# Kernel optimization log

Hardware: AMD Instinct MI355X
Metric: run time of the kernel (lower is better)

Reference implementation:

```python
import jax, jax.numpy as jnp
import numpy as np

NUM_CODES = 2048
CODE_DEPTH = 64
D_MODEL = 1024
EMA_DECAY = 0.99


def setup_inputs() -> dict:
    key = jax.random.key(0)
    ks = jax.random.split(key, 4)
    x = jax.random.normal(ks[0], (8, 2048, D_MODEL), dtype=jnp.float32)
    # downsampler Linear(d_model, code_depth)
    W_down = jax.random.normal(ks[1], (CODE_DEPTH, D_MODEL), dtype=jnp.float32) / np.sqrt(D_MODEL)
    b_down = jnp.zeros((CODE_DEPTH,), dtype=jnp.float32)
    # codebook: randn, row-normalized, code 0 zeroed (padding code)
    cb = jax.random.normal(ks[2], (1, NUM_CODES, CODE_DEPTH), dtype=jnp.float32)
    cb = cb / jnp.linalg.norm(cb, axis=-1, keepdims=True)
    cb = cb.at[:, 0].set(0.0)
    cluster_sizes = jnp.zeros((1, NUM_CODES), dtype=jnp.float32)
    cluster_sums = jnp.zeros((1, NUM_CODES, CODE_DEPTH), dtype=jnp.float32)
    return {"x": x, "W_down": W_down, "b_down": b_down, "codebook": cb,
            "cluster_sizes": cluster_sizes, "cluster_sums": cluster_sums}


def reference(x, W_down, b_down, codebook, cluster_sizes, cluster_sums):
    """Quantizer.forward, level=0, training=True, quantize=True, mask=None,
    gumbel=False, reverse_ema=False, ema_decay>0."""
    decay = EMA_DECAY
    num_codes = codebook.shape[1]
    cb = codebook[0]                                   # [K, D]
    # downsample + L2 normalize
    z = jnp.einsum('bsm,dm->bsd', x, W_down) + b_down  # [B, S, D]
    z = z / jnp.linalg.norm(z, axis=-1, keepdims=True)
    zd = jax.lax.stop_gradient(z)
    # cdist(z.detach(), codebook[1:]) -> euclidean distances [B, S, K-1]
    codes = cb[1:]
    d2 = (jnp.sum(zd * zd, -1, keepdims=True)
          + jnp.sum(codes * codes, -1)
          - 2.0 * jnp.einsum('bsd,kd->bsk', zd, codes))
    dist = jnp.sqrt(jnp.maximum(d2, 0.0))
    code_indices = jnp.argmin(dist, axis=-1) + 1       # [B, S], in [1, K)
    hard = cb[code_indices]                            # embedding lookup
    # commitment loss: mse(hard.detach(), z)
    commitment_loss = jnp.mean((jax.lax.stop_gradient(hard) - z) ** 2)
    # one-hot aggregation
    onehot = jax.nn.one_hot(code_indices, num_codes, dtype=z.dtype)  # [B,S,K]
    flat_onehot = onehot.reshape(-1, num_codes)        # [N, K]
    bincounts = flat_onehot.sum(axis=0)                # [K]
    used = bincounts != 0                              # [K] bool
    # unused-code loss: mean of per-(batch,code) min distance over unused codes
    code_dist = jnp.min(dist, axis=-2)                 # [B, K-1]
    unused_mask = ~used[1:]                            # [K-1]
    cnt = jnp.sum(unused_mask.astype(jnp.float32)) * code_dist.shape[0]
    unused_code_loss = jnp.sum(code_dist * unused_mask[None, :]) / jnp.maximum(cnt, 1.0)
    # EMA scatter update (forward/standard EMA)
    obs = zd.reshape(-1, zd.shape[-1])                 # [N, D]
    sums = flat_onehot.T @ obs                         # [K, D]
    new_cs = decay * cluster_sizes[0] + (1.0 - decay) * jax.lax.stop_gradient(bincounts)
    new_csum = decay * cluster_sums[0] + (1.0 - decay) * jax.lax.stop_gradient(sums)
    n = new_cs.sum()
    smoothed = (new_cs + 1e-5) * n / (n + num_codes * 1e-5)
    centroids = new_csum / smoothed[:, None]
    new_cb = jnp.where(used[:, None], jax.lax.stop_gradient(centroids), cb)
    new_cb = new_cb.at[0].set(0.0)
    # straight-through estimator
    hard_codes = z + jax.lax.stop_gradient(hard - z)
    embedding_loss = unused_code_loss
    return (hard_codes, code_indices, commitment_loss, embedding_loss,
            new_cb[None], new_cs[None], new_csum[None])
```

## Files before the change

kernel.cpp:

```cpp
#include <hip/hip_runtime.h>

#define NROWS 16384
#define DM    1024
#define CD    64
#define NC    2048
#define KC    2047
#define NB    8
#define DECAY 0.99f

#define K3_BLOCKS 512

#define OUT_HARD   0
#define OUT_IDX    1048576
#define OUT_COMMIT 1064960
#define OUT_EMB    1064961
#define OUT_CB     1064962
#define OUT_CS     1196034
#define OUT_CSUM   1198082

#define WS_Z      0
#define WS_CN2    1048576
#define WS_BINC   1050624
#define WS_SUMS   1052672
#define WS_CDIST  1183744
#define WS_COMMIT 1200120
#define WS_ZN2    1200632
#define WS_N      1217016
#define WS_PART   1298940
#define WS_BV     WS_PART
#define WS_BI     (WS_PART + 65536)

#define F32_INF_BITS 0x7F800000u

__global__ __launch_bounds__(256) void k0_init(const float* __restrict__ cb,
                                               float* __restrict__ ws) {
  int i = blockIdx.x * 256 + threadIdx.x;
  if (i < NC * CD) (ws + WS_SUMS)[i] = 0.0f;
  if (i < NC) {
    ((unsigned*)(ws + WS_BINC))[i] = 0u;
    float cn2;
    if (i < KC) {
      const float* c = cb + (size_t)(i + 1) * CD;
      float s0 = 0.f, s1 = 0.f;
      #pragma unroll
      for (int d = 0; d < CD; d += 2) { s0 = fmaf(c[d], c[d], s0); s1 = fmaf(c[d+1], c[d+1], s1); }
      cn2 = s0 + s1;
    } else {
      cn2 = __uint_as_float(F32_INF_BITS);
    }
    (ws + WS_CN2)[i] = cn2;
  }
  if (i < NB * KC) ((unsigned*)(ws + WS_CDIST))[i] = F32_INF_BITS;
}

__global__ __launch_bounds__(256) void k1_split(const float* __restrict__ x,
                                                const float* __restrict__ W,
                                                float* __restrict__ ws) {
  __shared__ float xs[64][132];
  __shared__ float wls[64][68];
  const int t = threadIdx.x;
  const int ks = blockIdx.x & 3;
  const int row0 = (blockIdx.x >> 2) * 128;
  const int kbase = ks * 256;
  const int tx = t & 15, ty = t >> 4;
  const int sseg = t & 15, srow = t >> 4;

  float4 px[8], pw[4];
  auto ld = [&](int kt) {
    const int kk = kbase + kt * 64;
    #pragma unroll
    for (int it = 0; it < 8; ++it)
      px[it] = *(const float4*)(x + (size_t)(row0 + srow + 16 * it) * DM + kk + sseg * 4);
    #pragma unroll
    for (int it = 0; it < 4; ++it)
      pw[it] = *(const float4*)(W + (size_t)(srow + 16 * it) * DM + kk + sseg * 4);
  };
  ld(0);

  float acc[8][4];
  #pragma unroll
  for (int i = 0; i < 8; i++)
    #pragma unroll
    for (int j = 0; j < 4; j++) acc[i][j] = 0.f;

  for (int kt = 0; kt < 4; ++kt) {
    __syncthreads();
    const int sg4 = sseg * 4;
    #pragma unroll
    for (int it = 0; it < 8; ++it) {
      const int cpos = (srow + 16 * it) ^ ((sseg & 3) << 3);
      xs[sg4 + 0][cpos] = px[it].x; xs[sg4 + 1][cpos] = px[it].y;
      xs[sg4 + 2][cpos] = px[it].z; xs[sg4 + 3][cpos] = px[it].w;
    }
    #pragma unroll
    for (int it = 0; it < 4; ++it) {
      const int wcol = srow + 16 * it;
      wls[sg4 + 0][wcol] = pw[it].x; wls[sg4 + 1][wcol] = pw[it].y;
      wls[sg4 + 2][wcol] = pw[it].z; wls[sg4 + 3][wcol] = pw[it].w;
    }
    __syncthreads();
    if (kt < 3) ld(kt + 1);

    #pragma unroll 8
    for (int dl = 0; dl < 64; ++dl) {
      const int xcol = (ty * 8) ^ (((dl >> 2) & 3) << 3);
      float4 xv0 = *(const float4*)(&xs[dl][xcol]);
      float4 xv1 = *(const float4*)(&xs[dl][xcol + 4]);
      float4 wv  = *(const float4*)(&wls[dl][tx * 4]);
      float xz[8] = {xv0.x, xv0.y, xv0.z, xv0.w, xv1.x, xv1.y, xv1.z, xv1.w};
      float wc[4] = {wv.x, wv.y, wv.z, wv.w};
      #pragma unroll
      for (int i = 0; i < 8; i++)
        #pragma unroll
        for (int j = 0; j < 4; j++)
          acc[i][j] = fmaf(xz[i], wc[j], acc[i][j]);
    }
  }

  float* part = ws + WS_PART + (size_t)ks * NROWS * CD;
  #pragma unroll
  for (int i = 0; i < 8; i++) {
    const int row = row0 + ty * 8 + i;
    float4 v; v.x = acc[i][0]; v.y = acc[i][1]; v.z = acc[i][2]; v.w = acc[i][3];
    *(float4*)(part + (size_t)row * CD + tx * 4) = v;
  }
}

__global__ __launch_bounds__(256) void k1_reduce(const float* __restrict__ bdown,
                                                 float* __restrict__ ws) {
  const int t = threadIdx.x;
  const int tx = t & 15, ty = t >> 4;
  const int row = blockIdx.x * 16 + ty;
  const float* part = ws + WS_PART;
  const size_t off = (size_t)row * CD + tx * 4;

  float4 v0 = *(const float4*)(part + off);
  float4 v1 = *(const float4*)(part + (size_t)1 * NROWS * CD + off);
  float4 v2 = *(const float4*)(part + (size_t)2 * NROWS * CD + off);
  float4 v3 = *(const float4*)(part + (size_t)3 * NROWS * CD + off);
  float4 b  = *(const float4*)(bdown + tx * 4);
  float4 v;
  v.x = (v0.x + v1.x) + (v2.x + v3.x) + b.x;
  v.y = (v0.y + v1.y) + (v2.y + v3.y) + b.y;
  v.z = (v0.z + v1.z) + (v2.z + v3.z) + b.z;
  v.w = (v0.w + v1.w) + (v2.w + v3.w) + b.w;

  float ss = v.x * v.x + v.y * v.y + v.z * v.z + v.w * v.w;
  #pragma unroll
  for (int m = 1; m < 16; m <<= 1) ss += __shfl_xor(ss, m, 64);
  float inv = 1.0f / sqrtf(ss);
  float4 zv; zv.x = v.x * inv; zv.y = v.y * inv; zv.z = v.z * inv; zv.w = v.w * inv;
  *(float4*)(ws + WS_Z + off) = zv;
  if (tx == 0) (ws + WS_ZN2)[row] = ss * inv * inv;
}

__global__ __launch_bounds__(256) void k1_down(const float* __restrict__ x,
                                               const float* __restrict__ W,
                                               const float* __restrict__ bdown,
                                               float* __restrict__ ws) {
  __shared__ float xs[64][68];
  __shared__ float wls[64][68];
  const int t = threadIdx.x;
  const int row0 = blockIdx.x * 64;
  const int tx = t & 15, ty = t >> 4;

  int pr[4], pseg[4];
  #pragma unroll
  for (int it = 0; it < 4; ++it) { int c = t + it * 256; pr[it] = c >> 4; pseg[it] = c & 15; }

  float4 px[4], pw[4];
  #pragma unroll
  for (int it = 0; it < 4; ++it) {
    px[it] = *(const float4*)(x + (size_t)(row0 + pr[it]) * DM + pseg[it] * 4);
    pw[it] = *(const float4*)(W + (size_t)pr[it] * DM + pseg[it] * 4);
  }

  float acc[4][4];
  #pragma unroll
  for (int i = 0; i < 4; i++)
    #pragma unroll
    for (int j = 0; j < 4; j++) acc[i][j] = 0.f;

  for (int kt = 0; kt < 16; ++kt) {
    __syncthreads();
    #pragma unroll
    for (int it = 0; it < 4; ++it) {
      *(float4*)(&xs[pr[it]][pseg[it] * 4]) = px[it];
      *(float4*)(&wls[pr[it]][pseg[it] * 4]) = pw[it];
    }
    __syncthreads();
    if (kt < 15) {
      const int k0 = (kt + 1) * 64;
      #pragma unroll
      for (int it = 0; it < 4; ++it) {
        px[it] = *(const float4*)(x + (size_t)(row0 + pr[it]) * DM + k0 + pseg[it] * 4);
        pw[it] = *(const float4*)(W + (size_t)pr[it] * DM + k0 + pseg[it] * 4);
      }
    }
    #pragma unroll 4
    for (int k = 0; k < 64; k += 4) {
      float4 xv[4], wv[4];
      #pragma unroll
      for (int i = 0; i < 4; i++) xv[i] = *(const float4*)(&xs[ty * 4 + i][k]);
      #pragma unroll
      for (int j = 0; j < 4; j++) wv[j] = *(const float4*)(&wls[tx * 4 + j][k]);
      #pragma unroll
      for (int i = 0; i < 4; i++)
        #pragma unroll
        for (int j = 0; j < 4; j++)
          acc[i][j] = fmaf(xv[i].x, wv[j].x, fmaf(xv[i].y, wv[j].y,
                      fmaf(xv[i].z, wv[j].z, fmaf(xv[i].w, wv[j].w, acc[i][j]))));
    }
  }

  #pragma unroll
  for (int j = 0; j < 4; j++) {
    float bj = bdown[tx * 4 + j];
    #pragma unroll
    for (int i = 0; i < 4; i++) acc[i][j] += bj;
  }

  float* z = ws + WS_Z;
  float* zn2 = ws + WS_ZN2;
  #pragma unroll
  for (int i = 0; i < 4; i++) {
    float ss = acc[i][0] * acc[i][0] + acc[i][1] * acc[i][1] +
               acc[i][2] * acc[i][2] + acc[i][3] * acc[i][3];
    #pragma unroll
    for (int m = 1; m < 16; m <<= 1) ss += __shfl_xor(ss, m, 64);
    float inv = 1.0f / sqrtf(ss);
    float4 zv;
    zv.x = acc[i][0] * inv; zv.y = acc[i][1] * inv;
    zv.z = acc[i][2] * inv; zv.w = acc[i][3] * inv;
    int row = row0 + ty * 4 + i;
    *(float4*)(z + (size_t)row * CD + tx * 4) = zv;
    if (tx == 0) zn2[row] = ss * inv * inv;
  }
}

__global__ __launch_bounds__(512) void k2_dist(const float* __restrict__ cbp,
                                               float* __restrict__ ws) {
  __shared__ float zT[64][132];
  __shared__ float cT[64][132];
  __shared__ float cn2s[128];
  __shared__ float zn2s[128];
  __shared__ unsigned colmin[128];

  const int t = threadIdx.x;
  const int gq = blockIdx.x & 3;
  const int rt = blockIdx.x >> 2;
  const int row0 = rt << 7;
  const int batch = rt >> 4;
  const int tx = t & 31, ty = t >> 5;
  const float* z = ws + WS_Z;
  const float* cn2p = ws + WS_CN2;
  unsigned* cdist = (unsigned*)(ws + WS_CDIST) + (size_t)batch * KC;

  if (t < 128) zn2s[t] = (ws + WS_ZN2)[row0 + t];

  {
    const int sr = t >> 2, sp = t & 3;
    float4 v[4];
    #pragma unroll
    for (int it = 0; it < 4; ++it)
      v[it] = *(const float4*)(z + (size_t)(row0 + sr) * CD + (sp + 4 * it) * 4);
    #pragma unroll
    for (int it = 0; it < 4; ++it) {
      const int sg4 = (sp + 4 * it) * 4;
      zT[sg4 + 0][sr] = v[it].x; zT[sg4 + 1][sr] = v[it].y;
      zT[sg4 + 2][sr] = v[it].z; zT[sg4 + 3][sr] = v[it].w;
    }
  }

  const int cr = t >> 2, cp = t & 3;
  const int ccol = cr ^ (((cr >> 5) & 3) << 2);
  float4 pc[4];
  auto ldc = [&](int lt) {
    const int code = gq * 512 + lt * 128 + cr;
    #pragma unroll
    for (int it = 0; it < 4; ++it)
      pc[it] = (code < KC) ? *(const float4*)(cbp + (size_t)(code + 1) * CD + (cp + 4 * it) * 4)
                           : make_float4(0.f, 0.f, 0.f, 0.f);
  };
  ldc(0);

  float bestv[8];
  int besti[8];
  #pragma unroll
  for (int i = 0; i < 8; i++) { bestv[i] = __uint_as_float(F32_INF_BITS); besti[i] = 0; }

  const int ccol0 = (tx * 4) ^ (((tx >> 3) & 3) << 2);

  for (int lt = 0; lt < 4; ++lt) {
    __syncthreads();
    #pragma unroll
    for (int it = 0; it < 4; ++it) {
      const int sg4 = (cp + 4 * it) * 4;
      cT[sg4 + 0][ccol] = pc[it].x; cT[sg4 + 1][ccol] = pc[it].y;
      cT[sg4 + 2][ccol] = pc[it].z; cT[sg4 + 3][ccol] = pc[it].w;
    }
    if (t < 128) {
      cn2s[t] = cn2p[gq * 512 + lt * 128 + t];
      colmin[t] = F32_INF_BITS;
    }
    __syncthreads();
    if (lt < 3) ldc(lt + 1);

    float acc[8][4];
    #pragma unroll
    for (int i = 0; i < 8; i++)
      #pragma unroll
      for (int j = 0; j < 4; j++) acc[i][j] = 0.f;

    #pragma unroll 8
    for (int d = 0; d < 64; ++d) {
      float4 za = *(const float4*)(&zT[d][ty * 8]);
      float4 zb = *(const float4*)(&zT[d][ty * 8 + 4]);
      float4 cv = *(const float4*)(&cT[d][ccol0]);
      float zz[8] = {za.x, za.y, za.z, za.w, zb.x, zb.y, zb.z, zb.w};
      float cc[4] = {cv.x, cv.y, cv.z, cv.w};
      #pragma unroll
      for (int i = 0; i < 8; i++)
        #pragma unroll
        for (int j = 0; j < 4; j++)
          acc[i][j] = fmaf(zz[i], cc[j], acc[i][j]);
    }

    const int jbase = gq * 512 + lt * 128;
    #pragma unroll
    for (int jl = 0; jl < 4; ++jl) {
      const int jloc = tx * 4 + jl;
      const int jg = jbase + jloc;
      const float c2 = cn2s[jloc];
      float colv = __uint_as_float(F32_INF_BITS);
      #pragma unroll
      for (int i = 0; i < 8; ++i) {
        float s = fmaf(-2.f, acc[i][jl], c2);
        if (s < bestv[i]) { bestv[i] = s; besti[i] = jg; }
        float v = zn2s[ty * 8 + i] + s;
        v = v < 0.f ? 0.f : v;
        colv = v < colv ? v : colv;
      }
      colv = fminf(colv, __shfl_xor(colv, 32, 64));
      if ((t & 32) == 0) atomicMin(&colmin[jloc], __float_as_uint(colv));
    }
    __syncthreads();
    if (t < 128) {
      const int jg2 = jbase + t;
      if (jg2 < KC) atomicMin(&cdist[jg2], colmin[t]);
    }
  }

  #pragma unroll
  for (int m = 1; m <= 16; m <<= 1) {
    #pragma unroll
    for (int i = 0; i < 8; i++) {
      float ov = __shfl_xor(bestv[i], m, 64);
      int oi = __shfl_xor(besti[i], m, 64);
      if (ov < bestv[i] || (ov == bestv[i] && oi < besti[i])) { bestv[i] = ov; besti[i] = oi; }
    }
  }
  if (tx == 0) {
    #pragma unroll
    for (int i = 0; i < 8; i++) {
      const int row = row0 + ty * 8 + i;
      (ws + WS_BV)[(size_t)gq * NROWS + row] = bestv[i];
      ((int*)(ws + WS_BI))[(size_t)gq * NROWS + row] = besti[i] + 1;
    }
  }
}

__global__ __launch_bounds__(256) void k3_scatter(const float* __restrict__ cb,
                                                  float* __restrict__ ws,
                                                  float* __restrict__ out) {
  const int t = threadIdx.x;
  const int lane = t & 63;
  const int w = t >> 6;
  const int rowbase = blockIdx.x * 32 + w * 8;
  const float* z = ws + WS_Z;

  const int myrow = rowbase + (lane & 7);
  float bv = (ws + WS_BV)[myrow];
  int myidx = ((const int*)(ws + WS_BI))[myrow];
  #pragma unroll
  for (int g2 = 1; g2 < 4; ++g2) {
    float v = (ws + WS_BV)[(size_t)g2 * NROWS + myrow];
    int i2 = ((const int*)(ws + WS_BI))[(size_t)g2 * NROWS + myrow];
    if (v < bv) { bv = v; myidx = i2; }
  }
  if (lane < 8) out[OUT_IDX + myrow] = (float)myidx;

  float sq = 0.f;
  #pragma unroll
  for (int r = 0; r < 8; ++r) {
    const int idx = __shfl(myidx, r, 8);
    const int row = rowbase + r;
    const float c = cb[(size_t)idx * CD + lane];
    const float zv = z[(size_t)row * CD + lane];
    out[OUT_HARD + (size_t)row * CD + lane] = zv + (c - zv);
    const float d = c - zv;
    sq = fmaf(d, d, sq);
    atomicAdd(ws + WS_SUMS + (size_t)idx * CD + lane, zv);
    if (lane == 0) atomicAdd((unsigned*)(ws + WS_BINC) + idx, 1u);
  }

  __shared__ float red[4];
  #pragma unroll
  for (int m = 1; m < 64; m <<= 1) sq += __shfl_xor(sq, m, 64);
  if (lane == 0) red[w] = sq;
  __syncthreads();
  if (t == 0) (ws + WS_COMMIT)[blockIdx.x] = red[0] + red[1] + red[2] + red[3];
}

__global__ __launch_bounds__(1024) void k4a_stats(const float* __restrict__ cs_in,
                                                  float* __restrict__ ws,
                                                  float* __restrict__ out) {
  __shared__ float red[1024];
  const int t = threadIdx.x;
  const unsigned* binc = (const unsigned*)(ws + WS_BINC);

  float npart = 0.f;
  #pragma unroll
  for (int i = t; i < NC; i += 1024) {
    float nc = DECAY * cs_in[i] + (1.f - DECAY) * (float)binc[i];
    out[OUT_CS + i] = nc;
    npart += nc;
  }
  red[t] = npart; __syncthreads();
  for (int s = 512; s > 0; s >>= 1) { if (t < s) red[t] += red[t + s]; __syncthreads(); }
  if (t == 0) (ws + WS_N)[0] = red[0];
  __syncthreads();

  float cpart = 0.f;
  for (int j = t; j < K3_BLOCKS; j += 1024) cpart += (ws + WS_COMMIT)[j];
  red[t] = cpart; __syncthreads();
  for (int s = 512; s > 0; s >>= 1) { if (t < s) red[t] += red[t + s]; __syncthreads(); }
  float commit = red[0]; __syncthreads();

  const unsigned* cdist = (const unsigned*)(ws + WS_CDIST);
  float lsum = 0.f, ccount = 0.f;
  for (int j = t; j < KC; j += 1024) {
    if (binc[j + 1] == 0u) {
      ccount += 1.f;
      float srow = 0.f;
      #pragma unroll
      for (int b = 0; b < NB; b++) srow += sqrtf(__uint_as_float(cdist[b * KC + j]));
      lsum += srow;
    }
  }
  red[t] = lsum; __syncthreads();
  for (int s = 512; s > 0; s >>= 1) { if (t < s) red[t] += red[t + s]; __syncthreads(); }
  float totloss = red[0]; __syncthreads();
  red[t] = ccount; __syncthreads();
  for (int s = 512; s > 0; s >>= 1) { if (t < s) red[t] += red[t + s]; __syncthreads(); }
  float cnt = red[0] * (float)NB;
  if (t == 0) {
    out[OUT_COMMIT] = commit / (float)(NROWS * CD);
    out[OUT_EMB] = totloss / fmaxf(cnt, 1.f);
  }
}

__global__ __launch_bounds__(256) void k4b_update(const float* __restrict__ cb,
                                                  const float* __restrict__ csum_in,
                                                  const float* __restrict__ ws,
                                                  float* __restrict__ out) {
  const int e = blockIdx.x * 256 + threadIdx.x;
  const int k = e >> 6;
  const unsigned* binc = (const unsigned*)(ws + WS_BINC);
  const float n = (ws + WS_N)[0];
  const float denom = n + (float)NC * 1e-5f;

  float ncsum = DECAY * csum_in[e] + (1.f - DECAY) * (ws + WS_SUMS)[e];
  out[OUT_CSUM + e] = ncsum;
  float smoothed = (out[OUT_CS + k] + 1e-5f) * n / denom;
  float cent = ncsum / smoothed;
  float v = (binc[k] != 0u) ? cent : cb[e];
  if (k == 0) v = 0.f;
  out[OUT_CB + e] = v;
}

extern "C" void kernel_launch(void* const* d_in, const int* in_sizes, int n_in,
                              void* d_out, int out_size, void* d_ws, size_t ws_size,
                              hipStream_t stream) {
  const float* x    = (const float*)d_in[0];
  const float* W    = (const float*)d_in[1];
  const float* b    = (const float*)d_in[2];
  const float* cb   = (const float*)d_in[3];
  const float* cs   = (const float*)d_in[4];
  const float* csum = (const float*)d_in[5];
  float* out = (float*)d_out;
  float* ws  = (float*)d_ws;

  const size_t need = ((size_t)WS_PART + (size_t)4 * NROWS * CD) * sizeof(float);
  const bool use_split = ws_size >= need;

  hipLaunchKernelGGL(k0_init, dim3(512), dim3(256), 0, stream, cb, ws);
  if (use_split) {
    hipLaunchKernelGGL(k1_split,  dim3(512),  dim3(256), 0, stream, x, W, ws);
    hipLaunchKernelGGL(k1_reduce, dim3(1024), dim3(256), 0, stream, b, ws);
  } else {
    hipLaunchKernelGGL(k1_down, dim3(256), dim3(256), 0, stream, x, W, b, ws);
  }
  hipLaunchKernelGGL(k2_dist,   dim3(512),       dim3(512),  0, stream, cb, ws);
  hipLaunchKernelGGL(k3_scatter,dim3(K3_BLOCKS), dim3(256),  0, stream, cb, ws, out);
  hipLaunchKernelGGL(k4a_stats, dim3(1),         dim3(1024), 0, stream, cs, ws, out);
  hipLaunchKernelGGL(k4b_update,dim3(512),       dim3(256),  0, stream, cb, csum, ws, out);
}
```

Measured before the change: 133.4 us.

## Use bf16 MFMA distance pass with top-3 candidates and fp32 rescoring

Replaces the fp32 shared-memory distance kernel with a bf16 MFMA kernel. Each row keeps its top-3 candidate codes per column lane, and a separate kernel rescores the candidates within a threshold in fp32 to pick the exact argmin. Per-batch code min distances are still accumulated with atomicMin, here from bf16 scores. This cuts the matmul cost of the distance search but adds conversion and rescore kernels, and the per-code minimum distances now carry bf16 error. Near-ties beyond the candidate set or threshold could also change the chosen index.

```diff
diff --git a/kernel.cpp b/kernel.cpp
--- a/kernel.cpp
+++ b/kernel.cpp
@@ -1,4 +1,5 @@
 #include <hip/hip_runtime.h>
+#include <hip/hip_bf16.h>
 
 #define NROWS 16384
 #define DM    1024
@@ -27,10 +28,22 @@
 #define WS_ZN2    1200632
 #define WS_N      1217016
 #define WS_PART   1298940
+#define WS_ZB2    WS_PART
+#define WS_CBB2   (WS_PART + 524288)
+#define WS_CAND   (WS_PART + 589824)
+#define WS_IDXM2  (WS_PART + 3735552)
 #define WS_BV     WS_PART
 #define WS_BI     (WS_PART + 65536)
 
 #define F32_INF_BITS 0x7F800000u
+
+typedef __attribute__((ext_vector_type(8))) short short8;
+typedef __attribute__((ext_vector_type(4))) float f32x4;
+
+__device__ inline unsigned short f2bf(float f) {
+  __hip_bfloat16 h = __float2bfloat16(f);
+  return *reinterpret_cast<unsigned short*>(&h);
+}
 
 __global__ __launch_bounds__(256) void k0_init(const float* __restrict__ cb,
                                                float* __restrict__ ws) {
@@ -238,6 +251,153 @@
   }
 }
 
+__global__ __launch_bounds__(256) void k_cvt(const float* __restrict__ cb,
+                                             float* __restrict__ ws) {
+  const int i = blockIdx.x * 256 + threadIdx.x;
+  unsigned short u[8];
+  if (i < NROWS * CD / 8) {
+    const float* src = ws + WS_Z + (size_t)i * 8;
+    #pragma unroll
+    for (int e = 0; e < 8; ++e) u[e] = f2bf(src[e]);
+    *(short8*)((unsigned short*)(ws + WS_ZB2) + (size_t)i * 8) = *(short8*)u;
+  } else if (i < NROWS * CD / 8 + NC * CD / 8) {
+    const int j = i - NROWS * CD / 8;
+    #pragma unroll
+    for (int e = 0; e < 8; ++e) {
+      const int f = j * 8 + e;
+      u[e] = (f < KC * CD) ? f2bf(cb[f + CD]) : (unsigned short)0;
+    }
+    *(short8*)((unsigned short*)(ws + WS_CBB2) + (size_t)j * 8) = *(short8*)u;
+  }
+}
+
+__global__ __launch_bounds__(64) void k2m_dist(float* __restrict__ ws) {
+  const int l = threadIdx.x;
+  const int half = blockIdx.x & 1;
+  const int rg = blockIdx.x >> 1;
+  const int row0 = rg * 16;
+  const int batch = row0 >> 11;
+  const unsigned short* zb = (const unsigned short*)(ws + WS_ZB2);
+  const unsigned short* cbb = (const unsigned short*)(ws + WS_CBB2);
+  const float* cn2p = ws + WS_CN2;
+  unsigned* cdist = (unsigned*)(ws + WS_CDIST) + (size_t)batch * KC;
+
+  const int col = l & 15, kb = l >> 4;
+  const size_t za = (size_t)(row0 + col) * CD + kb * 8;
+  short8 A0 = *(const short8*)(zb + za);
+  short8 A1 = *(const short8*)(zb + za + 32);
+
+  float zn2q[4];
+  #pragma unroll
+  for (int q = 0; q < 4; ++q) zn2q[q] = (ws + WS_ZN2)[row0 + kb * 4 + q];
+
+  float bv[4][3]; int bi[4][3];
+  #pragma unroll
+  for (int q = 0; q < 4; ++q)
+    #pragma unroll
+    for (int s = 0; s < 3; ++s) { bv[q][s] = __uint_as_float(F32_INF_BITS); bi[q][s] = KC; }
+
+  const int t0 = half * 64;
+  short8 B0, B1; float c2;
+  {
+    const size_t ca = (size_t)(t0 * 16 + col) * CD + kb * 8;
+    B0 = *(const short8*)(cbb + ca);
+    B1 = *(const short8*)(cbb + ca + 32);
+    c2 = cn2p[t0 * 16 + col];
+  }
+
+  for (int tt = 0; tt < 64; ++tt) {
+    const int tile = t0 + tt;
+    short8 nB0, nB1; float nc2 = 0.f;
+    if (tt < 63) {
+      const size_t ca = (size_t)((tile + 1) * 16 + col) * CD + kb * 8;
+      nB0 = *(const short8*)(cbb + ca);
+      nB1 = *(const short8*)(cbb + ca + 32);
+      nc2 = cn2p[(tile + 1) * 16 + col];
+    }
+    f32x4 acc = {0.f, 0.f, 0.f, 0.f};
+    acc = __builtin_amdgcn_mfma_f32_16x16x32_bf16(A0, B0, acc, 0, 0, 0);
+    acc = __builtin_amdgcn_mfma_f32_16x16x32_bf16(A1, B1, acc, 0, 0, 0);
+
+    const int code = tile * 16 + col;
+    float cmin = __uint_as_float(F32_INF_BITS);
+    #pragma unroll
+    for (int q = 0; q < 4; ++q) {
+      const float s = fmaf(-2.f, acc[q], c2);
+      if (s < bv[q][0]) {
+        bv[q][2] = bv[q][1]; bi[q][2] = bi[q][1];
+        bv[q][1] = bv[q][0]; bi[q][1] = bi[q][0];
+        bv[q][0] = s;        bi[q][0] = code;
+      } else if (s < bv[q][1]) {
+        bv[q][2] = bv[q][1]; bi[q][2] = bi[q][1];
+        bv[q][1] = s;        bi[q][1] = code;
+      } else if (s < bv[q][2]) {
+        bv[q][2] = s;        bi[q][2] = code;
+      }
+      float v = zn2q[q] + s;
+      v = v < 0.f ? 0.f : v;
+      cmin = v < cmin ? v : cmin;
+    }
+    cmin = fminf(cmin, __shfl_xor(cmin, 16, 64));
+    cmin = fminf(cmin, __shfl_xor(cmin, 32, 64));
+    if (l < 16 && code < KC) atomicMin(&cdist[code], __float_as_uint(cmin));
+    B0 = nB0; B1 = nB1; c2 = nc2;
+  }
+
+  float* cand = ws + WS_CAND;
+  #pragma unroll
+  for (int q = 0; q < 4; ++q) {
+    const int row = row0 + kb * 4 + q;
+    float* p = cand + (size_t)row * 192 + half * 96 + col * 6;
+    #pragma unroll
+    for (int s = 0; s < 3; ++s) {
+      float2 e; e.x = bv[q][s]; e.y = __int_as_float(bi[q][s]);
+      *(float2*)(p + s * 2) = e;
+    }
+  }
+}
+
+__global__ __launch_bounds__(256) void k2m_rescore(const float* __restrict__ cb,
+                                                   float* __restrict__ ws,
+                                                   float* __restrict__ out) {
+  const int row = blockIdx.x * 256 + threadIdx.x;
+  const float* cand = ws + WS_CAND + (size_t)row * 192;
+  float mn = __uint_as_float(F32_INF_BITS);
+  for (int s = 0; s < 96; ++s) mn = fminf(mn, cand[s * 2]);
+  const float thr = mn + 0.02f;
+
+  float zr[64];
+  {
+    const float* z = ws + WS_Z + (size_t)row * CD;
+    #pragma unroll
+    for (int c4 = 0; c4 < 16; ++c4) {
+      float4 v = *(const float4*)(z + c4 * 4);
+      zr[c4 * 4 + 0] = v.x; zr[c4 * 4 + 1] = v.y;
+      zr[c4 * 4 + 2] = v.z; zr[c4 * 4 + 3] = v.w;
+    }
+  }
+
+  float bestv = __uint_as_float(F32_INF_BITS);
+  int besti = 0x7FFFFFFF;
+  for (int s = 0; s < 96; ++s) {
+    const float v = cand[s * 2];
+    if (v <= thr) {
+      const int code = __float_as_int(cand[s * 2 + 1]);
+      if (code < KC) {
+        const float* c = cb + (size_t)(code + 1) * CD;
+        float dot = 0.f;
+        #pragma unroll
+        for (int d = 0; d < 64; ++d) dot = fmaf(zr[d], c[d], dot);
+        const float sc = fmaf(-2.f, dot, (ws + WS_CN2)[code]);
+        if (sc < bestv || (sc == bestv && code < besti)) { bestv = sc; besti = code; }
+      }
+    }
+  }
+  const int idx = besti + 1;
+  ((int*)(ws + WS_IDXM2))[row] = idx;
+  out[OUT_IDX + row] = (float)idx;
+}
+
 __global__ __launch_bounds__(512) void k2_dist(const float* __restrict__ cbp,
                                                float* __restrict__ ws) {
   __shared__ float zT[64][132];
@@ -368,6 +528,39 @@
       ((int*)(ws + WS_BI))[(size_t)gq * NROWS + row] = besti[i] + 1;
     }
   }
+}
+
+__global__ __launch_bounds__(256) void k3m_scatter(const float* __restrict__ cb,
+                                                   float* __restrict__ ws,
+                                                   float* __restrict__ out) {
+  const int t = threadIdx.x;
+  const int lane = t & 63;
+  const int w = t >> 6;
+  const int rowbase = blockIdx.x * 32 + w * 8;
+  const float* z = ws + WS_Z;
+
+  const int myidx = ((const int*)(ws + WS_IDXM2))[rowbase + (lane & 7)];
+
+  float sq = 0.f;
+  #pragma unroll
+  for (int r = 0; r < 8; ++r) {
+    const int idx = __shfl(myidx, r, 8);
+    const int row = rowbase + r;
+    const float c = cb[(size_t)idx * CD + lane];
+    const float zv = z[(size_t)row * CD + lane];
+    out[OUT_HARD + (size_t)row * CD + lane] = zv + (c - zv);
+    const float d = c - zv;
+    sq = fmaf(d, d, sq);
+    atomicAdd(ws + WS_SUMS + (size_t)idx * CD + lane, zv);
+    if (lane == 0) atomicAdd((unsigned*)(ws + WS_BINC) + idx, 1u);
+  }
+
+  __shared__ float red[4];
+  #pragma unroll
+  for (int m = 1; m < 64; m <<= 1) sq += __shfl_xor(sq, m, 64);
+  if (lane == 0) red[w] = sq;
+  __syncthreads();
+  if (t == 0) (ws + WS_COMMIT)[blockIdx.x] = red[0] + red[1] + red[2] + red[3];
 }
 
 __global__ __launch_bounds__(256) void k3_scatter(const float* __restrict__ cb,
@@ -498,11 +691,15 @@
   if (use_split) {
     hipLaunchKernelGGL(k1_split,  dim3(512),  dim3(256), 0, stream, x, W, ws);
     hipLaunchKernelGGL(k1_reduce, dim3(1024), dim3(256), 0, stream, b, ws);
+    hipLaunchKernelGGL(k_cvt,       dim3(576),       dim3(256), 0, stream, cb, ws);
+    hipLaunchKernelGGL(k2m_dist,    dim3(2048),      dim3(64),  0, stream, ws);
+    hipLaunchKernelGGL(k2m_rescore, dim3(64),        dim3(256), 0, stream, cb, ws, out);
+    hipLaunchKernelGGL(k3m_scatter, dim3(K3_BLOCKS), dim3(256), 0, stream, cb, ws, out);
   } else {
-    hipLaunchKernelGGL(k1_down, dim3(256), dim3(256), 0, stream, x, W, b, ws);
-  }
-  hipLaunchKernelGGL(k2_dist,   dim3(512),       dim3(512),  0, stream, cb, ws);
-  hipLaunchKernelGGL(k3_scatter,dim3(K3_BLOCKS), dim3(256),  0, stream, cb, ws, out);
-  hipLaunchKernelGGL(k4a_stats, dim3(1),         dim3(1024), 0, stream, cs, ws, out);
-  hipLaunchKernelGGL(k4b_update,dim3(512),       dim3(256),  0, stream, cb, csum, ws, out);
-}
+    hipLaunchKernelGGL(k1_down,    dim3(256),       dim3(256), 0, stream, x, W, b, ws);
+    hipLaunchKernelGGL(k2_dist,    dim3(512),       dim3(512), 0, stream, cb, ws);
+    hipLaunchKernelGGL(k3_scatter, dim3(K3_BLOCKS), dim3(256), 0, stream, cb, ws, out);
+  }
+  hipLaunchKernelGGL(k4a_stats,  dim3(1),   dim3(1024), 0, stream, cs, ws, out);
+  hipLaunchKernelGGL(k4b_update, dim3(512), dim3(256),  0, stream, cb, csum, ws, out);
+}
```

Measured after the change: 237.1 us. +77.8%, slower.
